# Kernel tuning notes

Hardware: AMD Instinct MI355X
Metric: run time of the kernel (lower is better)

## Reference

```python
import jax, jax.numpy as jnp
import numpy as np

B, N, D, H = 2, 2048, 1024, 16
HD = D // H  # 64
EPS = 1e-6


def setup_inputs() -> dict:
    key = jax.random.key(0)
    ks = jax.random.split(key, 16)
    rnd = lambda k, shp: jax.random.normal(k, shp, dtype=jnp.float32)
    w = lambda k, i, o: rnd(k, (i, o)) * 0.02  # stored as (in, out); y = x @ W
    return {
        "x": rnd(ks[0], (B, N, D)),
        "emb_B_D": rnd(ks[1], (B, D)),
        "gate": rnd(ks[2], (B, D)),
        "crossattn_emb": rnd(ks[3], (B, 128, D)),
        "rope_emb_L_1_1_D": rnd(ks[4], (N, HD)),
        "Wq1": w(ks[5], D, D), "Wq2": w(ks[6], D, D),
        "Wk1": w(ks[7], D, D), "Wk2": w(ks[8], D, D),
        "Wv": w(ks[9], D, D),
        "Wo": w(ks[10], D, D),
        "Wada1": w(ks[11], D, D),
        "Wada2": w(ks[12], D, 2 * D),
        "bada2": jnp.zeros((2 * D,), dtype=jnp.float32),
    }


def rotate_half(t):
    t1, t2 = jnp.split(t, 2, axis=-1)
    return jnp.concatenate([-t2, t1], axis=-1)


def reference(x, emb_B_D, gate, crossattn_emb, rope_emb_L_1_1_D,
              Wq1, Wq2, Wk1, Wk2, Wv, Wo, Wada1, Wada2, bada2):
    # adaLN modulation: SiLU -> Linear(no bias) -> Linear(bias)
    ada = jax.nn.silu(emb_B_D) @ Wada1 @ Wada2 + bada2          # [B, 2D]
    shift, scale = jnp.split(ada, 2, axis=1)                    # [B, D] each

    # LayerNorm (no affine) + scale/shift
    mu = jnp.mean(x, axis=-1, keepdims=True)
    var = jnp.var(x, axis=-1, keepdims=True)
    xn = (x - mu) * jax.lax.rsqrt(var + EPS)
    xn = xn * (1.0 + scale[:, None, :]) + shift[:, None, :]     # [B, N, D]

    # QKV projections (each to_q/to_k is two stacked linears, to_v one)
    q = xn @ Wq1 @ Wq2
    k = xn @ Wk1 @ Wk2
    v = xn @ Wv
    split_heads = lambda t: t.reshape(B, N, H, HD).transpose(0, 2, 1, 3)  # b h n d
    q, k, v = split_heads(q), split_heads(k), split_heads(v)

    # RoPE
    cos = jnp.cos(rope_emb_L_1_1_D)[None, None]                 # [1,1,N,HD]
    sin = jnp.sin(rope_emb_L_1_1_D)[None, None]
    q = q * cos + rotate_half(q) * sin
    k = k * cos + rotate_half(k) * sin

    # Attention
    sim = jnp.einsum("bhid,bhjd->bhij", q, k) * (HD ** -0.5)
    attn = jax.nn.softmax(sim, axis=-1)
    out = jnp.einsum("bhij,bhjd->bhid", attn, v)
    out = out.transpose(0, 2, 1, 3).reshape(B, N, D) @ Wo

    # Gated residual
    return x + gate[:, None, :] * out
```

## Files before the change

kernel.cpp:

```cpp
#include <hip/hip_runtime.h>
#include <stdint.h>
#include <math.h>

typedef unsigned short u16;
typedef __attribute__((ext_vector_type(8))) short short8;
typedef __attribute__((ext_vector_type(4))) float f32x4;
typedef __attribute__((ext_vector_type(4))) unsigned short u16x4;
typedef __attribute__((ext_vector_type(2))) unsigned int uint2v;

#define DEV static __device__ __forceinline__

DEV u16 f2bf(float f) {
    unsigned u = __builtin_bit_cast(unsigned, f);
    u = u + 0x7fffu + ((u >> 16) & 1u);
    return (u16)(u >> 16);
}
DEV float bf2f(u16 s) { return __builtin_bit_cast(float, ((unsigned)s) << 16); }
DEV unsigned pk2(float a, float b) {
    unsigned ua = __builtin_bit_cast(unsigned, a) + 0x8000u;
    unsigned ub = __builtin_bit_cast(unsigned, b) + 0x8000u;
    return (ua >> 16) | (ub & 0xffff0000u);
}
DEV float fexp2(float x) {
#if __has_builtin(__builtin_amdgcn_exp2f)
    return __builtin_amdgcn_exp2f(x);
#else
    return __expf(x * 0.69314718056f);
#endif
}

DEV void gl_lds16(const u16* g, u16* l) {
#if __has_builtin(__builtin_amdgcn_global_load_lds)
    __builtin_amdgcn_global_load_lds((const __attribute__((address_space(1))) unsigned int*)g,
                                     (__attribute__((address_space(3))) unsigned int*)l, 16, 0, 0);
#else
    *(short8*)l = *(const short8*)g;
#endif
}


__global__ __launch_bounds__(256) void k_ada1(const float* __restrict__ emb, const float* __restrict__ W,
                                              float* __restrict__ out) {
    int col = blockIdx.x * 64 + (threadIdx.x & 63);
    int b = blockIdx.y;
    int kseg = threadIdx.x >> 6;
    float acc = 0.f;
    for (int k = kseg * 256; k < kseg * 256 + 256; k++) {
        float e = emb[b * 1024 + k];
        float se = e / (1.f + __expf(-e));
        acc += se * W[(size_t)k * 1024 + col];
    }
    __shared__ float red[4][64];
    red[kseg][threadIdx.x & 63] = acc;
    __syncthreads();
    if (threadIdx.x < 64)
        out[b * 1024 + blockIdx.x * 64 + threadIdx.x] =
            red[0][threadIdx.x] + red[1][threadIdx.x] + red[2][threadIdx.x] + red[3][threadIdx.x];
}

__global__ __launch_bounds__(256) void k_prep(const float* s0, u16* d0, const float* s1, u16* d1,
                                              const float* s2, u16* d2, const float* s3, u16* d3,
                                              const float* s4, u16* d4, const float* s5, u16* d5,
                                              const float* __restrict__ t_ada, const float* __restrict__ Wada2,
                                              const float* __restrict__ bada2, float* __restrict__ ada,
                                              const float* __restrict__ rope,
                                              float* __restrict__ cst, float* __restrict__ snt) {
    __shared__ u16 tile[64][65];
    __shared__ float red[4][64];
    if (blockIdx.z == 6) {
        int flat = blockIdx.y * 16 + blockIdx.x;
        if (flat < 64) {
            int b = flat >> 5, xb = flat & 31;
            int col = xb * 64 + (threadIdx.x & 63);
            int kseg = threadIdx.x >> 6;
            float acc = 0.f;
            for (int k = kseg * 256; k < kseg * 256 + 256; k++)
                acc += t_ada[b * 1024 + k] * Wada2[(size_t)k * 2048 + col];
            red[kseg][threadIdx.x & 63] = acc;
            __syncthreads();
            if (threadIdx.x < 64) {
                int c = xb * 64 + threadIdx.x;
                ada[b * 2048 + c] = red[0][threadIdx.x] + red[1][threadIdx.x] +
                                    red[2][threadIdx.x] + red[3][threadIdx.x] + bada2[c];
            }
        } else if (flat < 192) {
            int idx = (flat - 64) * 1024 + threadIdx.x * 4;
            float4 rv = *(const float4*)(rope + idx);
            float4 cv, sv;
            __sincosf(rv.x, &sv.x, &cv.x);
            __sincosf(rv.y, &sv.y, &cv.y);
            __sincosf(rv.z, &sv.z, &cv.z);
            __sincosf(rv.w, &sv.w, &cv.w);
            *(float4*)(cst + idx) = cv;
            *(float4*)(snt + idx) = sv;
        }
        return;
    }
    const float* s; u16* d;
    switch (blockIdx.z) {
        case 0: s = s0; d = d0; break;
        case 1: s = s1; d = d1; break;
        case 2: s = s2; d = d2; break;
        case 3: s = s3; d = d3; break;
        case 4: s = s4; d = d4; break;
        default: s = s5; d = d5; break;
    }
    int k0 = blockIdx.x * 64, n0 = blockIdx.y * 64;
    int tx = threadIdx.x & 63, ty = threadIdx.x >> 6;
    if (blockIdx.z >= 4) {
        #pragma unroll
        for (int i = 0; i < 16; i++) {
            int kk = ty + 4 * i;
            d[(size_t)(k0 + kk) * 1024 + n0 + tx] = f2bf(s[(size_t)(k0 + kk) * 1024 + n0 + tx]);
        }
        return;
    }
    #pragma unroll
    for (int i = 0; i < 16; i++) {
        int kk = ty + 4 * i;
        tile[kk][tx] = f2bf(s[(size_t)(k0 + kk) * 1024 + n0 + tx]);
    }
    __syncthreads();
    #pragma unroll
    for (int i = 0; i < 16; i++) {
        int nn = ty + 4 * i;
        d[(size_t)(n0 + nn) * 1024 + k0 + tx] = tile[tx][nn];
    }
}

__global__ __launch_bounds__(256) void k_ln(const float* __restrict__ x, const float* __restrict__ ada,
                                            u16* __restrict__ xn) {
    int row = blockIdx.x;
    int b = row >> 11;
    float4 v = ((const float4*)(x + (size_t)row * 1024))[threadIdx.x];
    float s = v.x + v.y + v.z + v.w;
    float ss = v.x * v.x + v.y * v.y + v.z * v.z + v.w * v.w;
    #pragma unroll
    for (int m = 1; m < 64; m <<= 1) { s += __shfl_xor(s, m, 64); ss += __shfl_xor(ss, m, 64); }
    __shared__ float red[2][4];
    int wave = threadIdx.x >> 6, lane = threadIdx.x & 63;
    if (lane == 0) { red[0][wave] = s; red[1][wave] = ss; }
    __syncthreads();
    s = red[0][0] + red[0][1] + red[0][2] + red[0][3];
    ss = red[1][0] + red[1][1] + red[1][2] + red[1][3];
    float mu = s * (1.f / 1024.f);
    float var = ss * (1.f / 1024.f) - mu * mu;
    float rs = rsqrtf(var + 1e-6f);
    int c = threadIdx.x * 4;
    const float* sh = ada + b * 2048;
    const float* sc = ada + b * 2048 + 1024;
    u16x4 r;
    r.x = f2bf((v.x - mu) * rs * (1.f + sc[c + 0]) + sh[c + 0]);
    r.y = f2bf((v.y - mu) * rs * (1.f + sc[c + 1]) + sh[c + 1]);
    r.z = f2bf((v.z - mu) * rs * (1.f + sc[c + 2]) + sh[c + 2]);
    r.w = f2bf((v.w - mu) * rs * (1.f + sc[c + 3]) + sh[c + 3]);
    *(u16x4*)(xn + (size_t)row * 1024 + c) = r;
}

template <int BM, int BN, int MODE>
DEV void gemm_core(const u16* __restrict__ A, const u16* __restrict__ Bt,
                   u16* __restrict__ Cb, float* __restrict__ Cf, u16* __restrict__ Vt,
                   const float* __restrict__ Xres, const float* __restrict__ gate,
                   const float* __restrict__ cst, const float* __restrict__ snt,
                   float scale, int Nn, int K, int m0, int n0) {
    constexpr int MI = BM / 32, NJ = BN / 32;
    __shared__ u16 As[2][BM][64];
    __shared__ u16 Bs[2][BN][64];
    int tid = threadIdx.x;
    int lane = tid & 63, wave = tid >> 6;
    int wm = (wave & 1) * (BM / 2), wn = (wave >> 1) * (BN / 2);
    int lr = lane & 15, quad = lane >> 4;
    f32x4 acc[MI][NJ];
    #pragma unroll
    for (int i = 0; i < MI; i++)
        #pragma unroll
        for (int j = 0; j < NJ; j++) acc[i][j] = f32x4{0.f, 0.f, 0.f, 0.f};

    int arow = tid >> 3;
    int acol = (tid & 7) * 8;
    int g8 = (((tid & 7) ^ (arow & 7))) * 8;
    int cc[2] = { ((quad ^ (lr & 7))) * 8, (((4 + quad) ^ (lr & 7))) * 8 };

    const u16* ap = A + (size_t)(m0 + arow) * K + g8;
    const u16* bp = Bt + (size_t)(n0 + arow) * K + g8;

    short8 ra[2][MI], rb[2][NJ];
    #pragma unroll
    for (int p = 0; p < MI; p++) ra[0][p] = *(const short8*)(ap + (size_t)(32 * p) * K);
    #pragma unroll
    for (int p = 0; p < NJ; p++) rb[0][p] = *(const short8*)(bp + (size_t)(32 * p) * K);
    #pragma unroll
    for (int p = 0; p < MI; p++) *(short8*)(&As[0][arow + 32 * p][acol]) = ra[0][p];
    #pragma unroll
    for (int p = 0; p < NJ; p++) *(short8*)(&Bs[0][arow + 32 * p][acol]) = rb[0][p];
    #pragma unroll
    for (int p = 0; p < MI; p++) ra[1][p] = *(const short8*)(ap + 64 + (size_t)(32 * p) * K);
    #pragma unroll
    for (int p = 0; p < NJ; p++) rb[1][p] = *(const short8*)(bp + 64 + (size_t)(32 * p) * K);
    __syncthreads();

    auto body = [&](int it, int cur) {
        if (it + 2 < 16) {
            const u16* aq = ap + (size_t)(it + 2) * 64;
            const u16* bq = bp + (size_t)(it + 2) * 64;
            #pragma unroll
            for (int p = 0; p < MI; p++) ra[cur][p] = *(const short8*)(aq + (size_t)(32 * p) * K);
            #pragma unroll
            for (int p = 0; p < NJ; p++) rb[cur][p] = *(const short8*)(bq + (size_t)(32 * p) * K);
        }
        #pragma unroll
        for (int ks = 0; ks < 2; ks++) {
            short8 af[MI], bfr[NJ];
            #pragma unroll
            for (int i = 0; i < MI; i++) af[i] = *(const short8*)(&As[cur][wm + i * 16 + lr][cc[ks]]);
            #pragma unroll
            for (int j = 0; j < NJ; j++) bfr[j] = *(const short8*)(&Bs[cur][wn + j * 16 + lr][cc[ks]]);
            #pragma unroll
            for (int i = 0; i < MI; i++)
                #pragma unroll
                for (int j = 0; j < NJ; j++)
                    acc[i][j] = __builtin_amdgcn_mfma_f32_16x16x32_bf16(af[i], bfr[j], acc[i][j], 0, 0, 0);
        }
        if (it + 1 < 16) {
            int nxt = cur ^ 1;
            #pragma unroll
            for (int p = 0; p < MI; p++) *(short8*)(&As[nxt][arow + 32 * p][acol]) = ra[nxt][p];
            #pragma unroll
            for (int p = 0; p < NJ; p++) *(short8*)(&Bs[nxt][arow + 32 * p][acol]) = rb[nxt][p];
        }
        __syncthreads();
    };
    #pragma unroll 1
    for (int it2 = 0; it2 < 8; ++it2) {
        body(2 * it2, 0);
        body(2 * it2 + 1, 1);
    }

    if (MODE == 2) {
        if ((n0 + wn) < 2048) {
            #pragma unroll
            for (int i = 0; i < MI; i++)
                #pragma unroll
                for (int jp = 0; jp < 2; jp++)
                    #pragma unroll
                    for (int r = 0; r < 4; r++) {
                        int row = m0 + wm + i * 16 + quad * 4 + r;
                        int n = row & 2047;
                        int d1 = jp * 16 + lr;
                        float c1 = cst[n * 64 + d1],      s1 = snt[n * 64 + d1];
                        float c2 = cst[n * 64 + d1 + 32], s2 = snt[n * 64 + d1 + 32];
                        float x1 = acc[i][jp][r], x2 = acc[i][jp + 2][r];
                        Cb[(size_t)row * Nn + n0 + wn + d1]      = f2bf(x1 * c1 - x2 * s1);
                        Cb[(size_t)row * Nn + n0 + wn + d1 + 32] = f2bf(x2 * c2 + x1 * s2);
                    }
        } else {
            int hv = (n0 + wn - 2048) >> 6;
            #pragma unroll
            for (int i = 0; i < MI; i++)
                #pragma unroll
                for (int j = 0; j < NJ; j++) {
                    int token = m0 + wm + i * 16 + quad * 4;
                    int bb = token >> 11;
                    int nloc = token & 2047;
                    u16x4 w;
                    w.x = f2bf(acc[i][j][0]); w.y = f2bf(acc[i][j][1]);
                    w.z = f2bf(acc[i][j][2]); w.w = f2bf(acc[i][j][3]);
                    *(u16x4*)(Vt + ((size_t)((bb * 16 + hv) * 64 + j * 16 + lr)) * 2048 + nloc) = w;
                }
        }
        return;
    }
    #pragma unroll
    for (int i = 0; i < MI; i++)
        #pragma unroll
        for (int j = 0; j < NJ; j++)
            #pragma unroll
            for (int r = 0; r < 4; r++) {
                int row = m0 + wm + i * 16 + quad * 4 + r;
                int col = n0 + wn + j * 16 + lr;
                float v = acc[i][j][r];
                if (MODE == 1) {
                    int b = row >> 11;
                    Cf[(size_t)row * Nn + col] = Xres[(size_t)row * Nn + col] + gate[b * 1024 + col] * v;
                } else {
                    Cb[(size_t)row * Nn + col] = f2bf(v * scale);
                }
            }
}

template <int BM, int BN, int MODE, int WPE>
__global__ __launch_bounds__(256, WPE) void gemm_bt(const u16* __restrict__ A, const u16* __restrict__ Bt,
                                                    u16* __restrict__ Cb, float* __restrict__ Cf,
                                                    u16* __restrict__ Vt,
                                                    const float* __restrict__ Xres, const float* __restrict__ gate,
                                                    const float* __restrict__ cst, const float* __restrict__ snt,
                                                    int Nn, int K) {
    gemm_core<BM, BN, MODE>(A, Bt, Cb, Cf, Vt, Xres, gate, cst, snt, 1.f, Nn, K,
                            blockIdx.y * BM, blockIdx.x * BN);
}

__global__ __launch_bounds__(256, 4) void gemm_fold(const u16* A0, const u16* B0, u16* C0,
                                                    const u16* A1, const u16* B1, u16* C1) {
    const u16* A = blockIdx.z ? A1 : A0;
    const u16* Bt = blockIdx.z ? B1 : B0;
    u16* C = blockIdx.z ? C1 : C0;
    float scale = blockIdx.z ? 1.0f : 0.18033688f;
    gemm_core<64, 64, 0>(A, Bt, C, nullptr, nullptr, nullptr, nullptr, nullptr, nullptr, scale,
                         1024, 1024, blockIdx.y * 64, blockIdx.x * 64);
}

__global__ __launch_bounds__(256) void k_attn(const u16* __restrict__ qkv, const u16* __restrict__ vt,
                                              u16* __restrict__ dump, float* __restrict__ paL) {
    __shared__ u16 pool[128 * 72];
    __shared__ u16 Ks[2][64][64];
    __shared__ u16 Vs[2][64][64];
    int q0 = blockIdx.x * 128;
    int bh = blockIdx.y; int b = bh >> 4, h = bh & 15;
    int z = blockIdx.z;
    int kbase = z * 1024;
    int tid = threadIdx.x;
    int lane = tid & 63, wave = tid >> 6;
    int lr = lane & 15, quad = lane >> 4;
    int srow = tid >> 3, scol = (tid & 7) * 8;
    int sg = (((tid & 7) ^ (srow & 7))) * 8;
    int cc[2] = { ((quad ^ (lr & 7))) * 8, (((4 + quad) ^ (lr & 7))) * 8 };

    const u16* kp = qkv + ((size_t)(b * 2048 + kbase + srow)) * 2048 + 1024 + h * 64 + sg;
    const u16* vp = vt + ((size_t)(bh * 64 + srow)) * 2048 + kbase + sg;

    #pragma unroll
    for (int p = 0; p < 4; p++)
        gl_lds16(qkv + ((size_t)(b * 2048 + q0 + srow + 32 * p)) * 2048 + h * 64 + sg,
                 pool + (srow + 32 * p) * 64 + scol);

    short8 krA[2], vrA[2], krB[2], vrB[2];
    krA[0] = *(const short8*)(kp);               krA[1] = *(const short8*)(kp + (size_t)32 * 2048);
    vrA[0] = *(const short8*)(vp);               vrA[1] = *(const short8*)(vp + (size_t)32 * 2048);
    __syncthreads();
    short8 qf[2][2];
    #pragma unroll
    for (int rt = 0; rt < 2; rt++)
        #pragma unroll
        for (int ks = 0; ks < 2; ks++)
            qf[rt][ks] = *(const short8*)(pool + (wave * 32 + rt * 16 + lr) * 64 + cc[ks]);
    *(short8*)(&Ks[0][srow][scol])      = krA[0];
    *(short8*)(&Ks[0][srow + 32][scol]) = krA[1];
    *(short8*)(&Vs[0][srow][scol])      = vrA[0];
    *(short8*)(&Vs[0][srow + 32][scol]) = vrA[1];
    krB[0] = *(const short8*)(kp + (size_t)64 * 2048);  krB[1] = *(const short8*)(kp + (size_t)96 * 2048);
    vrB[0] = *(const short8*)(vp + 64);                 vrB[1] = *(const short8*)(vp + 64 + (size_t)32 * 2048);
    __syncthreads();

    float l_part[2] = {0.f, 0.f};
    f32x4 oacc[2][4];
    #pragma unroll
    for (int rt = 0; rt < 2; rt++)
        #pragma unroll
        for (int dt = 0; dt < 4; dt++) oacc[rt][dt] = f32x4{0.f, 0.f, 0.f, 0.f};

    auto body = [&](int it, int cur, short8 (&krF)[2], short8 (&vrF)[2],
                    short8 (&krH)[2], short8 (&vrH)[2]) {
        if (it < 14) {
            const u16* kq = kp + (size_t)(it + 2) * 64 * 2048;
            const u16* vq = vp + (it + 2) * 64;
            krF[0] = *(const short8*)(kq);  krF[1] = *(const short8*)(kq + (size_t)32 * 2048);
            vrF[0] = *(const short8*)(vq);  vrF[1] = *(const short8*)(vq + (size_t)32 * 2048);
        }
        f32x4 st[2][4];
        #pragma unroll
        for (int rt = 0; rt < 2; rt++)
            #pragma unroll
            for (int ct = 0; ct < 4; ct++) st[rt][ct] = f32x4{0.f, 0.f, 0.f, 0.f};
        #pragma unroll
        for (int ks = 0; ks < 2; ks++) {
            short8 kf[4];
            #pragma unroll
            for (int ct = 0; ct < 4; ct++)
                kf[ct] = *(const short8*)(&Ks[cur][ct * 16 + lr][cc[ks]]);
            #pragma unroll
            for (int rt = 0; rt < 2; rt++)
                #pragma unroll
                for (int ct = 0; ct < 4; ct++)
                    st[rt][ct] = __builtin_amdgcn_mfma_f32_16x16x32_bf16(kf[ct], qf[rt][ks], st[rt][ct], 0, 0, 0);
        }
        #pragma unroll
        for (int rt = 0; rt < 2; rt++)
            #pragma unroll
            for (int ct = 0; ct < 4; ct++) {
                float p0 = fexp2(st[rt][ct][0]);
                float p1 = fexp2(st[rt][ct][1]);
                float p2 = fexp2(st[rt][ct][2]);
                float p3 = fexp2(st[rt][ct][3]);
                l_part[rt] += (p0 + p1) + (p2 + p3);
                uint2v w; w.x = pk2(p0, p1); w.y = pk2(p2, p3);
                *(uint2v*)(pool + (wave * 32 + rt * 16 + lr) * 72 + ct * 16 + quad * 4) = w;
            }
        #pragma unroll
        for (int ks = 0; ks < 2; ks++) {
            short8 pf[2], vf[4];
            #pragma unroll
            for (int rt = 0; rt < 2; rt++)
                pf[rt] = *(const short8*)(pool + (wave * 32 + rt * 16 + lr) * 72 + ks * 32 + quad * 8);
            #pragma unroll
            for (int dt = 0; dt < 4; dt++)
                vf[dt] = *(const short8*)(&Vs[cur][dt * 16 + lr][cc[ks]]);
            #pragma unroll
            for (int rt = 0; rt < 2; rt++)
                #pragma unroll
                for (int dt = 0; dt < 4; dt++)
                    oacc[rt][dt] = __builtin_amdgcn_mfma_f32_16x16x32_bf16(pf[rt], vf[dt], oacc[rt][dt], 0, 0, 0);
        }
        if (it < 15) {
            int nxt = cur ^ 1;
            *(short8*)(&Ks[nxt][srow][scol])      = krH[0];
            *(short8*)(&Ks[nxt][srow + 32][scol]) = krH[1];
            *(short8*)(&Vs[nxt][srow][scol])      = vrH[0];
            *(short8*)(&Vs[nxt][srow + 32][scol]) = vrH[1];
        }
        __syncthreads();
    };

    #pragma unroll 1
    for (int it2 = 0; it2 < 8; ++it2) {
        body(2 * it2,     0, krA, vrA, krB, vrB);
        body(2 * it2 + 1, 1, krB, vrB, krA, vrA);
    }

    #pragma unroll
    for (int rt = 0; rt < 2; rt++) {
        float l = l_part[rt];
        l += __shfl_xor(l, 16, 64);
        l += __shfl_xor(l, 32, 64);
        if (quad == 0)
            paL[(size_t)z * 65536 + bh * 2048 + q0 + wave * 32 + rt * 16 + lr] = l;
    }
    u16* dp = dump + (size_t)z * 4194304 + ((size_t)(bh * 16 + blockIdx.x) * 256 + tid) * 32;
    #pragma unroll
    for (int rt = 0; rt < 2; rt++)
        #pragma unroll
        for (int dt = 0; dt < 4; dt++) {
            u16x4 w;
            w.x = f2bf(oacc[rt][dt][0]); w.y = f2bf(oacc[rt][dt][1]);
            w.z = f2bf(oacc[rt][dt][2]); w.w = f2bf(oacc[rt][dt][3]);
            *(u16x4*)(dp + rt * 16 + dt * 4) = w;
        }
}

__global__ __launch_bounds__(256) void k_comb(const u16* __restrict__ dump, const float* __restrict__ paL,
                                              u16* __restrict__ aob) {
    int bx = blockIdx.x, bh = blockIdx.y;
    int b = bh >> 4, h = bh & 15;
    int tid = threadIdx.x;
    int lane = tid & 63, wave = tid >> 6;
    int lr = lane & 15, quad = lane >> 4;
    int q0 = bx * 128;
    const u16* d0 = dump + ((size_t)(bh * 16 + bx) * 256 + tid) * 32;
    const u16* d1 = d0 + 4194304;
    #pragma unroll
    for (int rt = 0; rt < 2; rt++) {
        float inv[4];
        #pragma unroll
        for (int r = 0; r < 4; r++) {
            int row = q0 + wave * 32 + rt * 16 + quad * 4 + r;
            float l0 = paL[bh * 2048 + row];
            float l1 = paL[65536 + bh * 2048 + row];
            inv[r] = 1.f / (l0 + l1);
        }
        #pragma unroll
        for (int dt = 0; dt < 4; dt++) {
            u16x4 w0 = *(const u16x4*)(d0 + rt * 16 + dt * 4);
            u16x4 w1 = *(const u16x4*)(d1 + rt * 16 + dt * 4);
            #pragma unroll
            for (int r = 0; r < 4; r++) {
                int row = q0 + wave * 32 + rt * 16 + quad * 4 + r;
                float o = (bf2f(((const u16*)&w0)[r]) + bf2f(((const u16*)&w1)[r])) * inv[r];
                aob[((size_t)(b * 2048 + row)) * 1024 + h * 64 + dt * 16 + lr] = f2bf(o);
            }
        }
    }
}

extern "C" void kernel_launch(void* const* d_in, const int* in_sizes, int n_in,
                              void* d_out, int out_size, void* d_ws, size_t ws_size,
                              hipStream_t stream) {
    const float* x     = (const float*)d_in[0];
    const float* emb   = (const float*)d_in[1];
    const float* gate  = (const float*)d_in[2];
    const float* rope  = (const float*)d_in[4];
    const float* Wq1   = (const float*)d_in[5];
    const float* Wq2   = (const float*)d_in[6];
    const float* Wk1   = (const float*)d_in[7];
    const float* Wk2   = (const float*)d_in[8];
    const float* Wv    = (const float*)d_in[9];
    const float* Wo    = (const float*)d_in[10];
    const float* Wada1 = (const float*)d_in[11];
    const float* Wada2 = (const float*)d_in[12];
    const float* bada2 = (const float*)d_in[13];
    float* out = (float*)d_out;

    char* ws = (char*)d_ws;
    size_t off = 0;
    auto alloc = [&](size_t bytes) { void* p = ws + off; off += (bytes + 255) & ~(size_t)255; return p; };
    float* t_ada = (float*)alloc(2048 * 4);
    float* ada   = (float*)alloc(4096 * 4);
    float* cst   = (float*)alloc((size_t)131072 * 4);
    float* snt   = (float*)alloc((size_t)131072 * 4);
    u16* xn    = (u16*)alloc((size_t)4096 * 1024 * 2);
    u16* Wq1b  = (u16*)alloc((size_t)1024 * 1024 * 2);
    u16* Wk1b  = (u16*)alloc((size_t)1024 * 1024 * 2);
    u16* Wq2t  = (u16*)alloc((size_t)1024 * 1024 * 2);
    u16* Wk2t  = (u16*)alloc((size_t)1024 * 1024 * 2);
    u16* Wot   = (u16*)alloc((size_t)1024 * 1024 * 2);
    u16* WqkvT = (u16*)alloc((size_t)3072 * 1024 * 2);
    u16* qkvb  = (u16*)alloc((size_t)4096 * 2048 * 2);
    u16* vtb   = (u16*)alloc((size_t)4096 * 1024 * 2);
    u16* aob   = (u16*)alloc((size_t)4096 * 1024 * 2);
    u16* dumpO = (u16*)alloc((size_t)2 * 4194304 * 2);
    float* paL = (float*)alloc((size_t)2 * 65536 * 4);
    (void)ws_size; (void)in_sizes; (void)n_in; (void)out_size;

    k_ada1<<<dim3(16, 2), 256, 0, stream>>>(emb, Wada1, t_ada);

    k_prep<<<dim3(16, 16, 7), 256, 0, stream>>>(Wq2, Wq2t, Wk2, Wk2t,
                                                Wv, WqkvT + (size_t)2048 * 1024, Wo, Wot,
                                                Wq1, Wq1b, Wk1, Wk1b,
                                                t_ada, Wada2, bada2, ada, rope, cst, snt);

    k_ln<<<4096, 256, 0, stream>>>(x, ada, xn);

    gemm_fold<<<dim3(16, 16, 2), 256, 0, stream>>>(Wq2t, Wq1b, WqkvT,
                                                   Wk2t, Wk1b, WqkvT + (size_t)1024 * 1024);

    gemm_bt<128, 128, 2, 2><<<dim3(24, 32), 256, 0, stream>>>(xn, WqkvT, qkvb, nullptr, vtb,
                                                              nullptr, nullptr, cst, snt, 2048, 1024);

    k_attn<<<dim3(16, 32, 2), 256, 0, stream>>>(qkvb, vtb, dumpO, paL);
    k_comb<<<dim3(16, 32), 256, 0, stream>>>(dumpO, paL, aob);

    gemm_bt<128, 64, 1, 3><<<dim3(16, 32), 256, 0, stream>>>(aob, Wot, nullptr, out, nullptr, x, gate,
                                                             nullptr, nullptr, 1024, 1024);
}
```

Measured before the change: 279.8 us.

## Split ada GEMVs with atomics, retile GEMM core to BK=32, stage V transpose in LDS

The adaLN GEMVs are split over more blocks along K and reduced with atomicAdd, using memsets to zero the outputs. The bias add moves into the LayerNorm kernel. The shared GEMM core switches from 64-wide K tiles with XOR swizzling to 32-wide K tiles with padded rows of stride 40, and doubles the iteration count. The V output is transposed through LDS so stores are coalesced, and occupancy hints and the fold GEMM tile size change. These changes aim for more parallelism in the small GEMVs and better coalescing, at the cost of more barriers per K step and nondeterministic atomic summation.

```diff
diff --git a/kernel.cpp b/kernel.cpp
--- a/kernel.cpp
+++ b/kernel.cpp
@@ -43,48 +43,50 @@
                                               float* __restrict__ out) {
     int col = blockIdx.x * 64 + (threadIdx.x & 63);
     int b = blockIdx.y;
-    int kseg = threadIdx.x >> 6;
+    int kbase = blockIdx.z * 128 + (threadIdx.x >> 6) * 32;
     float acc = 0.f;
-    for (int k = kseg * 256; k < kseg * 256 + 256; k++) {
+    for (int k = kbase; k < kbase + 32; k++) {
         float e = emb[b * 1024 + k];
         float se = e / (1.f + __expf(-e));
         acc += se * W[(size_t)k * 1024 + col];
     }
     __shared__ float red[4][64];
-    red[kseg][threadIdx.x & 63] = acc;
+    red[threadIdx.x >> 6][threadIdx.x & 63] = acc;
     __syncthreads();
     if (threadIdx.x < 64)
-        out[b * 1024 + blockIdx.x * 64 + threadIdx.x] =
-            red[0][threadIdx.x] + red[1][threadIdx.x] + red[2][threadIdx.x] + red[3][threadIdx.x];
+        atomicAdd(out + b * 1024 + blockIdx.x * 64 + threadIdx.x,
+                  red[0][threadIdx.x] + red[1][threadIdx.x] + red[2][threadIdx.x] + red[3][threadIdx.x]);
 }
 
 __global__ __launch_bounds__(256) void k_prep(const float* s0, u16* d0, const float* s1, u16* d1,
                                               const float* s2, u16* d2, const float* s3, u16* d3,
                                               const float* s4, u16* d4, const float* s5, u16* d5,
                                               const float* __restrict__ t_ada, const float* __restrict__ Wada2,
-                                              const float* __restrict__ bada2, float* __restrict__ ada,
-                                              const float* __restrict__ rope,
+                                              float* __restrict__ ada, const float* __restrict__ rope,
                                               float* __restrict__ cst, float* __restrict__ snt) {
     __shared__ u16 tile[64][65];
     __shared__ float red[4][64];
     if (blockIdx.z == 6) {
         int flat = blockIdx.y * 16 + blockIdx.x;
-        if (flat < 64) {
-            int b = flat >> 5, xb = flat & 31;
-            int col = xb * 64 + (threadIdx.x & 63);
-            int kseg = threadIdx.x >> 6;
-            float acc = 0.f;
-            for (int k = kseg * 256; k < kseg * 256 + 256; k++)
-                acc += t_ada[b * 1024 + k] * Wada2[(size_t)k * 2048 + col];
-            red[kseg][threadIdx.x & 63] = acc;
-            __syncthreads();
-            if (threadIdx.x < 64) {
-                int c = xb * 64 + threadIdx.x;
-                ada[b * 2048 + c] = red[0][threadIdx.x] + red[1][threadIdx.x] +
-                                    red[2][threadIdx.x] + red[3][threadIdx.x] + bada2[c];
-            }
-        } else if (flat < 192) {
-            int idx = (flat - 64) * 1024 + threadIdx.x * 4;
+        int kq = flat >> 6;
+        int rest = flat & 63;
+        int b = rest >> 5, xb = rest & 31;
+        int col = xb * 64 + (threadIdx.x & 63);
+        int kbase = kq * 256 + (threadIdx.x >> 6) * 64;
+        float acc = 0.f;
+        for (int k = kbase; k < kbase + 64; k++)
+            acc += t_ada[b * 1024 + k] * Wada2[(size_t)k * 2048 + col];
+        red[threadIdx.x >> 6][threadIdx.x & 63] = acc;
+        __syncthreads();
+        if (threadIdx.x < 64)
+            atomicAdd(ada + b * 2048 + xb * 64 + threadIdx.x,
+                      red[0][threadIdx.x] + red[1][threadIdx.x] + red[2][threadIdx.x] + red[3][threadIdx.x]);
+        return;
+    }
+    if (blockIdx.z == 7) {
+        int flat = blockIdx.y * 16 + blockIdx.x;
+        if (flat < 128) {
+            int idx = flat * 1024 + threadIdx.x * 4;
             float4 rv = *(const float4*)(rope + idx);
             float4 cv, sv;
             __sincosf(rv.x, &sv.x, &cv.x);
@@ -129,7 +131,7 @@
 }
 
 __global__ __launch_bounds__(256) void k_ln(const float* __restrict__ x, const float* __restrict__ ada,
-                                            u16* __restrict__ xn) {
+                                            const float* __restrict__ bada2, u16* __restrict__ xn) {
     int row = blockIdx.x;
     int b = row >> 11;
     float4 v = ((const float4*)(x + (size_t)row * 1024))[threadIdx.x];
@@ -150,10 +152,10 @@
     const float* sh = ada + b * 2048;
     const float* sc = ada + b * 2048 + 1024;
     u16x4 r;
-    r.x = f2bf((v.x - mu) * rs * (1.f + sc[c + 0]) + sh[c + 0]);
-    r.y = f2bf((v.y - mu) * rs * (1.f + sc[c + 1]) + sh[c + 1]);
-    r.z = f2bf((v.z - mu) * rs * (1.f + sc[c + 2]) + sh[c + 2]);
-    r.w = f2bf((v.w - mu) * rs * (1.f + sc[c + 3]) + sh[c + 3]);
+    r.x = f2bf((v.x - mu) * rs * (1.f + sc[c + 0] + bada2[1024 + c + 0]) + sh[c + 0] + bada2[c + 0]);
+    r.y = f2bf((v.y - mu) * rs * (1.f + sc[c + 1] + bada2[1024 + c + 1]) + sh[c + 1] + bada2[c + 1]);
+    r.z = f2bf((v.z - mu) * rs * (1.f + sc[c + 2] + bada2[1024 + c + 2]) + sh[c + 2] + bada2[c + 2]);
+    r.w = f2bf((v.w - mu) * rs * (1.f + sc[c + 3] + bada2[1024 + c + 3]) + sh[c + 3] + bada2[c + 3]);
     *(u16x4*)(xn + (size_t)row * 1024 + c) = r;
 }
 
@@ -164,8 +166,9 @@
                    const float* __restrict__ cst, const float* __restrict__ snt,
                    float scale, int Nn, int K, int m0, int n0) {
     constexpr int MI = BM / 32, NJ = BN / 32;
-    __shared__ u16 As[2][BM][64];
-    __shared__ u16 Bs[2][BN][64];
+    constexpr int PA = BM / 64, PB = BN / 64;
+    constexpr int LA = BM * 40, LB = BN * 40;
+    __shared__ u16 smem[2 * (LA + LB)];
     int tid = threadIdx.x;
     int lane = tid & 63, wave = tid >> 6;
     int wm = (wave & 1) * (BM / 2), wn = (wave >> 1) * (BN / 2);
@@ -176,62 +179,57 @@
         #pragma unroll
         for (int j = 0; j < NJ; j++) acc[i][j] = f32x4{0.f, 0.f, 0.f, 0.f};
 
-    int arow = tid >> 3;
-    int acol = (tid & 7) * 8;
-    int g8 = (((tid & 7) ^ (arow & 7))) * 8;
-    int cc[2] = { ((quad ^ (lr & 7))) * 8, (((4 + quad) ^ (lr & 7))) * 8 };
-
-    const u16* ap = A + (size_t)(m0 + arow) * K + g8;
-    const u16* bp = Bt + (size_t)(n0 + arow) * K + g8;
-
-    short8 ra[2][MI], rb[2][NJ];
-    #pragma unroll
-    for (int p = 0; p < MI; p++) ra[0][p] = *(const short8*)(ap + (size_t)(32 * p) * K);
-    #pragma unroll
-    for (int p = 0; p < NJ; p++) rb[0][p] = *(const short8*)(bp + (size_t)(32 * p) * K);
-    #pragma unroll
-    for (int p = 0; p < MI; p++) *(short8*)(&As[0][arow + 32 * p][acol]) = ra[0][p];
-    #pragma unroll
-    for (int p = 0; p < NJ; p++) *(short8*)(&Bs[0][arow + 32 * p][acol]) = rb[0][p];
-    #pragma unroll
-    for (int p = 0; p < MI; p++) ra[1][p] = *(const short8*)(ap + 64 + (size_t)(32 * p) * K);
-    #pragma unroll
-    for (int p = 0; p < NJ; p++) rb[1][p] = *(const short8*)(bp + 64 + (size_t)(32 * p) * K);
+    int arow = tid >> 2;
+    int achunk = (tid & 3) * 8;
+    const u16* ap = A + (size_t)(m0 + arow) * K + achunk;
+    const u16* bp = Bt + (size_t)(n0 + arow) * K + achunk;
+    u16* AsL[2] = { smem, smem + LA };
+    u16* BsL[2] = { smem + 2 * LA, smem + 2 * LA + LB };
+
+    short8 ra[2][PA], rb[2][PB];
+    #pragma unroll
+    for (int p = 0; p < PA; p++) ra[0][p] = *(const short8*)(ap + (size_t)(64 * p) * K);
+    #pragma unroll
+    for (int p = 0; p < PB; p++) rb[0][p] = *(const short8*)(bp + (size_t)(64 * p) * K);
+    #pragma unroll
+    for (int p = 0; p < PA; p++) *(short8*)(&AsL[0][(arow + 64 * p) * 40 + achunk]) = ra[0][p];
+    #pragma unroll
+    for (int p = 0; p < PB; p++) *(short8*)(&BsL[0][(arow + 64 * p) * 40 + achunk]) = rb[0][p];
+    #pragma unroll
+    for (int p = 0; p < PA; p++) ra[1][p] = *(const short8*)(ap + 32 + (size_t)(64 * p) * K);
+    #pragma unroll
+    for (int p = 0; p < PB; p++) rb[1][p] = *(const short8*)(bp + 32 + (size_t)(64 * p) * K);
     __syncthreads();
 
     auto body = [&](int it, int cur) {
-        if (it + 2 < 16) {
-            const u16* aq = ap + (size_t)(it + 2) * 64;
-            const u16* bq = bp + (size_t)(it + 2) * 64;
-            #pragma unroll
-            for (int p = 0; p < MI; p++) ra[cur][p] = *(const short8*)(aq + (size_t)(32 * p) * K);
-            #pragma unroll
-            for (int p = 0; p < NJ; p++) rb[cur][p] = *(const short8*)(bq + (size_t)(32 * p) * K);
-        }
-        #pragma unroll
-        for (int ks = 0; ks < 2; ks++) {
-            short8 af[MI], bfr[NJ];
-            #pragma unroll
-            for (int i = 0; i < MI; i++) af[i] = *(const short8*)(&As[cur][wm + i * 16 + lr][cc[ks]]);
-            #pragma unroll
-            for (int j = 0; j < NJ; j++) bfr[j] = *(const short8*)(&Bs[cur][wn + j * 16 + lr][cc[ks]]);
-            #pragma unroll
-            for (int i = 0; i < MI; i++)
-                #pragma unroll
-                for (int j = 0; j < NJ; j++)
-                    acc[i][j] = __builtin_amdgcn_mfma_f32_16x16x32_bf16(af[i], bfr[j], acc[i][j], 0, 0, 0);
-        }
-        if (it + 1 < 16) {
+        if (it + 2 < 32) {
+            int koff = (it + 2) * 32;
+            #pragma unroll
+            for (int p = 0; p < PA; p++) ra[cur][p] = *(const short8*)(ap + koff + (size_t)(64 * p) * K);
+            #pragma unroll
+            for (int p = 0; p < PB; p++) rb[cur][p] = *(const short8*)(bp + koff + (size_t)(64 * p) * K);
+        }
+        short8 af[MI], bfr[NJ];
+        #pragma unroll
+        for (int i = 0; i < MI; i++) af[i] = *(const short8*)(&AsL[cur][(wm + i * 16 + lr) * 40 + quad * 8]);
+        #pragma unroll
+        for (int j = 0; j < NJ; j++) bfr[j] = *(const short8*)(&BsL[cur][(wn + j * 16 + lr) * 40 + quad * 8]);
+        #pragma unroll
+        for (int i = 0; i < MI; i++)
+            #pragma unroll
+            for (int j = 0; j < NJ; j++)
+                acc[i][j] = __builtin_amdgcn_mfma_f32_16x16x32_bf16(af[i], bfr[j], acc[i][j], 0, 0, 0);
+        if (it + 1 < 32) {
             int nxt = cur ^ 1;
             #pragma unroll
-            for (int p = 0; p < MI; p++) *(short8*)(&As[nxt][arow + 32 * p][acol]) = ra[nxt][p];
-            #pragma unroll
-            for (int p = 0; p < NJ; p++) *(short8*)(&Bs[nxt][arow + 32 * p][acol]) = rb[nxt][p];
+            for (int p = 0; p < PA; p++) *(short8*)(&AsL[nxt][(arow + 64 * p) * 40 + achunk]) = ra[nxt][p];
+            #pragma unroll
+            for (int p = 0; p < PB; p++) *(short8*)(&BsL[nxt][(arow + 64 * p) * 40 + achunk]) = rb[nxt][p];
         }
         __syncthreads();
     };
     #pragma unroll 1
-    for (int it2 = 0; it2 < 8; ++it2) {
+    for (int it2 = 0; it2 < 16; ++it2) {
         body(2 * it2, 0);
         body(2 * it2 + 1, 1);
     }
@@ -254,19 +252,25 @@
                         Cb[(size_t)row * Nn + n0 + wn + d1 + 32] = f2bf(x2 * c2 + x1 * s2);
                     }
         } else {
-            int hv = (n0 + wn - 2048) >> 6;
             #pragma unroll
             for (int i = 0; i < MI; i++)
                 #pragma unroll
                 for (int j = 0; j < NJ; j++) {
-                    int token = m0 + wm + i * 16 + quad * 4;
-                    int bb = token >> 11;
-                    int nloc = token & 2047;
                     u16x4 w;
                     w.x = f2bf(acc[i][j][0]); w.y = f2bf(acc[i][j][1]);
                     w.z = f2bf(acc[i][j][2]); w.w = f2bf(acc[i][j][3]);
-                    *(u16x4*)(Vt + ((size_t)((bb * 16 + hv) * 64 + j * 16 + lr)) * 2048 + nloc) = w;
+                    *(u16x4*)(&smem[(wn + j * 16 + lr) * 132 + wm + i * 16 + quad * 4]) = w;
                 }
+            __syncthreads();
+            int d = tid >> 1, half = tid & 1;
+            int gcol = n0 - 2048 + d;
+            int hv = gcol >> 6, dl = gcol & 63;
+            int bb = m0 >> 11;
+            int nloc = (m0 & 2047) + half * 64;
+            u16* dst = Vt + ((size_t)((bb * 16 + hv) * 64 + dl)) * 2048 + nloc;
+            #pragma unroll
+            for (int c = 0; c < 8; c++)
+                *(short8*)(dst + c * 8) = *(const short8*)(&smem[d * 132 + half * 64 + c * 8]);
         }
         return;
     }
@@ -305,8 +309,8 @@
     const u16* Bt = blockIdx.z ? B1 : B0;
     u16* C = blockIdx.z ? C1 : C0;
     float scale = blockIdx.z ? 1.0f : 0.18033688f;
-    gemm_core<64, 64, 0>(A, Bt, C, nullptr, nullptr, nullptr, nullptr, nullptr, nullptr, scale,
-                         1024, 1024, blockIdx.y * 64, blockIdx.x * 64);
+    gemm_core<128, 64, 0>(A, Bt, C, nullptr, nullptr, nullptr, nullptr, nullptr, nullptr, scale,
+                          1024, 1024, blockIdx.y * 128, blockIdx.x * 64);
 }
 
 __global__ __launch_bounds__(256) void k_attn(const u16* __restrict__ qkv, const u16* __restrict__ vt,
@@ -519,24 +523,27 @@
     float* paL = (float*)alloc((size_t)2 * 65536 * 4);
     (void)ws_size; (void)in_sizes; (void)n_in; (void)out_size;
 
-    k_ada1<<<dim3(16, 2), 256, 0, stream>>>(emb, Wada1, t_ada);
-
-    k_prep<<<dim3(16, 16, 7), 256, 0, stream>>>(Wq2, Wq2t, Wk2, Wk2t,
+    hipMemsetAsync(t_ada, 0, 2048 * 4, stream);
+    hipMemsetAsync(ada, 0, 4096 * 4, stream);
+
+    k_ada1<<<dim3(16, 2, 8), 256, 0, stream>>>(emb, Wada1, t_ada);
+
+    k_prep<<<dim3(16, 16, 8), 256, 0, stream>>>(Wq2, Wq2t, Wk2, Wk2t,
                                                 Wv, WqkvT + (size_t)2048 * 1024, Wo, Wot,
                                                 Wq1, Wq1b, Wk1, Wk1b,
-                                                t_ada, Wada2, bada2, ada, rope, cst, snt);
-
-    k_ln<<<4096, 256, 0, stream>>>(x, ada, xn);
-
-    gemm_fold<<<dim3(16, 16, 2), 256, 0, stream>>>(Wq2t, Wq1b, WqkvT,
-                                                   Wk2t, Wk1b, WqkvT + (size_t)1024 * 1024);
-
-    gemm_bt<128, 128, 2, 2><<<dim3(24, 32), 256, 0, stream>>>(xn, WqkvT, qkvb, nullptr, vtb,
+                                                t_ada, Wada2, ada, rope, cst, snt);
+
+    k_ln<<<4096, 256, 0, stream>>>(x, ada, bada2, xn);
+
+    gemm_fold<<<dim3(16, 8, 2), 256, 0, stream>>>(Wq2t, Wq1b, WqkvT,
+                                                  Wk2t, Wk1b, WqkvT + (size_t)1024 * 1024);
+
+    gemm_bt<128, 128, 2, 3><<<dim3(24, 32), 256, 0, stream>>>(xn, WqkvT, qkvb, nullptr, vtb,
                                                               nullptr, nullptr, cst, snt, 2048, 1024);
 
     k_attn<<<dim3(16, 32, 2), 256, 0, stream>>>(qkvb, vtb, dumpO, paL);
     k_comb<<<dim3(16, 32), 256, 0, stream>>>(dumpO, paL, aob);
 
-    gemm_bt<128, 64, 1, 3><<<dim3(16, 32), 256, 0, stream>>>(aob, Wot, nullptr, out, nullptr, x, gate,
+    gemm_bt<128, 64, 1, 4><<<dim3(16, 32), 256, 0, stream>>>(aob, Wot, nullptr, out, nullptr, x, gate,
                                                              nullptr, nullptr, 1024, 1024);
 }
```

Result: faster. 273.6 us (-2.2%).
